# Performance work log

Measured on AMD Instinct MI355X. Metric: run time of the kernel, lower is better.

Reference implementation:

```python
import jax, jax.numpy as jnp
import numpy as np

EMBED_DIM = 1024
NUM_HEADS = 16
HEAD_DIM = EMBED_DIM // NUM_HEADS


def setup_inputs() -> dict:
    key = jax.random.key(0)
    ks = jax.random.split(key, 9)
    B, S, E, Hd = 1, 4096, EMBED_DIM, HEAD_DIM
    s = 0.02
    return {
        "x": jax.random.normal(ks[0], (B, S, E), jnp.float32),
        "mask": jnp.ones((B, S, S), jnp.int32),
        "Wq": jax.random.normal(ks[1], (E, E), jnp.float32) * s,
        "bq": jnp.zeros((E,), jnp.float32),
        "Wk": jax.random.normal(ks[2], (E, Hd), jnp.float32) * s,
        "bk": jnp.zeros((Hd,), jnp.float32),
        "Wv": jax.random.normal(ks[3], (E, Hd), jnp.float32) * s,
        "bv": jnp.zeros((Hd,), jnp.float32),
        "Wo": jax.random.normal(ks[4], (E, E), jnp.float32) * s,
        "bo": jnp.zeros((E,), jnp.float32),
    }


def reference(x, mask, Wq, bq, Wk, bk, Wv, bv, Wo, bo):
    B, S, E = x.shape
    H, Hd = NUM_HEADS, HEAD_DIM
    q = (x @ Wq + bq).reshape(B, S, H, Hd).transpose(0, 2, 1, 3)  # [B,H,S,Hd]
    k = x @ Wk + bk  # [B,S,Hd] single KV head (MQA)
    v = x @ Wv + bv  # [B,S,Hd]
    scale = 1.0 / np.sqrt(Hd).astype(np.float32)
    # broadcast single-head K across all query heads
    qk = jnp.einsum('bhqd,bkd->bhqk', q, k) * scale  # [B,H,S,S]
    qk = jnp.where(mask[:, None, :, :] == 0, jnp.float32(-10000.0), qk)
    attn = jax.nn.softmax(qk, axis=-1)
    out = jnp.einsum('bhqk,bkd->bhqd', attn, v)  # [B,H,S,Hd]
    out = out.transpose(0, 2, 1, 3).reshape(B, S, E)
    return out @ Wo + bo
```

## Files before the change

kernel.cpp:

```cpp
#include <hip/hip_runtime.h>
#include <hip/hip_bf16.h>
#include <stdint.h>

typedef __bf16 bf16x8 __attribute__((ext_vector_type(8)));
typedef float f32x4 __attribute__((ext_vector_type(4)));
typedef float f32x16 __attribute__((ext_vector_type(16)));
typedef unsigned int uint2v __attribute__((ext_vector_type(2)));

#define E_DIM 1024
#define HD 64
#define NH 16
#define QKV_LD 1152
#define LOG2E 1.44269504088896f

__device__ __forceinline__ float toF(float x) { return x; }
__device__ __forceinline__ float toF(__hip_bfloat16 x) { return __bfloat162float(x); }
__device__ __forceinline__ void storeOut(float* p, float v) { *p = v; }
__device__ __forceinline__ void storeOut(__hip_bfloat16* p, float v) { *p = __float2bfloat16(v); }

__device__ __forceinline__ unsigned cvtpk_bf16(float lo, float hi_) {
    unsigned r;
    asm("v_cvt_pk_bf16_f32 %0, %1, %2" : "=v"(r) : "v"(lo), "v"(hi_));
    return r;
}
__device__ __forceinline__ void perm32swap(unsigned& a, unsigned& b) {
    uint2v r = __builtin_amdgcn_permlane32_swap(a, b, false, false);
    a = r.x; b = r.y;
}
__device__ __forceinline__ float fexp2(float x) {
    float r;
    asm("v_exp_f32 %0, %1" : "=v"(r) : "v"(x));
    return r;
}

typedef __attribute__((address_space(1))) void gvoid;
typedef __attribute__((address_space(3))) void lvoid;
__device__ __forceinline__ void gload_lds16(const void* g, void* l) {
    __builtin_amdgcn_global_load_lds((gvoid*)g, (lvoid*)l, 16, 0, 0);
}

__global__ void cast_f32_bf16_kernel(const float* __restrict__ in, __hip_bfloat16* __restrict__ o, int n) {
    int i = (blockIdx.x * blockDim.x + threadIdx.x) * 4;
    if (i + 3 < n) {
        float4 v = *reinterpret_cast<const float4*>(in + i);
        __hip_bfloat16 t[4] = {__float2bfloat16(v.x), __float2bfloat16(v.y),
                               __float2bfloat16(v.z), __float2bfloat16(v.w)};
        *reinterpret_cast<uint2*>(o + i) = *reinterpret_cast<uint2*>(t);
    }
}

template<typename InT>
__global__ void transpose_cast_kernel(const InT* __restrict__ in, int ldi,
                                      __hip_bfloat16* __restrict__ out, int ldo,
                                      int R, int C) {
    __shared__ float tile[32][33];
    const int bx = blockIdx.x * 32;
    const int by = blockIdx.y * 32;
    const int tx = threadIdx.x & 31, ty = threadIdx.x >> 5;
#pragma unroll
    for (int j = 0; j < 4; ++j) {
        int r = bx + ty + j * 8, c = by + tx;
        tile[ty + j * 8][tx] = toF(in[(size_t)r * ldi + c]);
    }
    __syncthreads();
#pragma unroll
    for (int j = 0; j < 4; ++j) {
        int c = by + ty + j * 8, r = bx + tx;
        out[(size_t)c * ldo + r] = __float2bfloat16(tile[tx][ty + j * 8]);
    }
}

__global__ __launch_bounds__(256)
void transpose4_kernel(const float* __restrict__ Wq, const float* __restrict__ Wk,
                       const float* __restrict__ Wv, const float* __restrict__ Wo,
                       __hip_bfloat16* __restrict__ wqkvT, __hip_bfloat16* __restrict__ woT) {
    const int z = blockIdx.z;
    const float* in; __hip_bfloat16* out; int ldi;
    if (z == 0)      { in = Wq; out = wqkvT;                                ldi = E_DIM; }
    else if (z == 1) { if (blockIdx.y >= HD / 32) return;
                       in = Wk; out = wqkvT + (size_t)E_DIM * E_DIM;        ldi = HD; }
    else if (z == 2) { if (blockIdx.y >= HD / 32) return;
                       in = Wv; out = wqkvT + (size_t)(E_DIM + HD) * E_DIM; ldi = HD; }
    else             { in = Wo; out = woT;                                  ldi = E_DIM; }
    __shared__ float tile[32][33];
    const int bx = blockIdx.x * 32;
    const int by = blockIdx.y * 32;
    const int tx = threadIdx.x & 31, ty = threadIdx.x >> 5;
#pragma unroll
    for (int j = 0; j < 4; ++j) {
        int r = bx + ty + j * 8, c = by + tx;
        tile[ty + j * 8][tx] = in[(size_t)r * ldi + c];
    }
    __syncthreads();
#pragma unroll
    for (int j = 0; j < 4; ++j) {
        int c = by + ty + j * 8, r = bx + tx;
        out[(size_t)c * E_DIM + r] = __float2bfloat16(tile[tx][ty + j * 8]);
    }
}

__global__ void concat_bias3_kernel(const float* __restrict__ bq, const float* __restrict__ bk,
                                    const float* __restrict__ bv, float* __restrict__ bqkv) {
    int i = blockIdx.x * blockDim.x + threadIdx.x;
    if (i < E_DIM) bqkv[i] = bq[i];
    else if (i < E_DIM + HD) bqkv[i] = bk[i - E_DIM];
    else if (i < E_DIM + 2 * HD) bqkv[i] = bv[i - E_DIM - HD];
}

__global__ void maskbits_kernel(const int* __restrict__ mask, unsigned long long* __restrict__ mb,
                                int nwords) {
    int gtid = blockIdx.x * blockDim.x + threadIdx.x;
    int wid = gtid >> 6, lane = gtid & 63;
    int nw = (gridDim.x * blockDim.x) >> 6;
    for (int w = wid; w < nwords; w += nw) {
        int v = mask[(size_t)w * 64 + lane];
        unsigned long long b = __ballot(v != 0);
        if (lane == 0) mb[w] = b;
    }
}

template<typename OutT>
__global__ __launch_bounds__(256)
void gemm_bt3_kernel(const __hip_bfloat16* __restrict__ A,
                     const __hip_bfloat16* __restrict__ Bt,
                     const float* __restrict__ bias,
                     OutT* __restrict__ C,
                     int M, int N, int K, float sQ, int nQ, float sKV) {
    constexpr int BM = 64, BN = 128, BK = 64;
    __shared__ __align__(16) unsigned char lA[2][BM * BK * 2];
    __shared__ __align__(16) unsigned char lB[2][BN * BK * 2];
    const int ntn = N / BN;
    const int tm = blockIdx.x / ntn, tn = blockIdx.x % ntn;
    const int tid = threadIdx.x, lane = tid & 63, wave = tid >> 6;
    const int l15 = lane & 15, l4 = lane >> 4;
    const int wm = (wave >> 1) * 32, wn = (wave & 1) * 64;
    const int r0 = tm * BM, c0 = tn * BN;
    const int NK = K / BK;

    size_t aoff[2]; unsigned ldsoA[2];
    size_t boff[4]; unsigned ldsoB[4];
#pragma unroll
    for (int i = 0; i < 2; ++i) {
        int row = wave * 16 + i * 8 + (lane >> 3);
        int c = (lane & 7) ^ (row & 7);
        aoff[i] = (size_t)(r0 + row) * K * 2 + c * 16;
        ldsoA[i] = wave * 2048 + i * 1024;
    }
#pragma unroll
    for (int i = 0; i < 4; ++i) {
        int row = wave * 32 + i * 8 + (lane >> 3);
        int c = (lane & 7) ^ (row & 7);
        boff[i] = (size_t)(c0 + row) * K * 2 + c * 16;
        ldsoB[i] = wave * 4096 + i * 1024;
    }
    const char* Ab = (const char*)A;
    const char* Bb = (const char*)Bt;

#pragma unroll
    for (int i = 0; i < 2; ++i) gload_lds16(Ab + aoff[i], &lA[0][ldsoA[i]]);
#pragma unroll
    for (int i = 0; i < 4; ++i) gload_lds16(Bb + boff[i], &lB[0][ldsoB[i]]);
    __syncthreads();

    f32x4 z4 = {0.f, 0.f, 0.f, 0.f};
    f32x4 acc[2][4];
#pragma unroll
    for (int mi = 0; mi < 2; ++mi)
#pragma unroll
        for (int ni = 0; ni < 4; ++ni) acc[mi][ni] = z4;

    int buf = 0;
    for (int ks = 0; ks < NK; ++ks) {
        if (ks + 1 < NK) {
            size_t kb = (size_t)(ks + 1) * BK * 2;
#pragma unroll
            for (int i = 0; i < 2; ++i) gload_lds16(Ab + aoff[i] + kb, &lA[buf ^ 1][ldsoA[i]]);
#pragma unroll
            for (int i = 0; i < 4; ++i) gload_lds16(Bb + boff[i] + kb, &lB[buf ^ 1][ldsoB[i]]);
        }
        bf16x8 af[2][2], bf[4][2];
#pragma unroll
        for (int mi = 0; mi < 2; ++mi) {
            int row = wm + mi * 16 + l15;
#pragma unroll
            for (int kh = 0; kh < 2; ++kh) {
                int slot = (kh * 4 + l4) ^ (row & 7);
                af[mi][kh] = *reinterpret_cast<const bf16x8*>(&lA[buf][row * 128 + slot * 16]);
            }
        }
#pragma unroll
        for (int ni = 0; ni < 4; ++ni) {
            int row = wn + ni * 16 + l15;
#pragma unroll
            for (int kh = 0; kh < 2; ++kh) {
                int slot = (kh * 4 + l4) ^ (row & 7);
                bf[ni][kh] = *reinterpret_cast<const bf16x8*>(&lB[buf][row * 128 + slot * 16]);
            }
        }
        __builtin_amdgcn_s_setprio(1);
#pragma unroll
        for (int mi = 0; mi < 2; ++mi)
#pragma unroll
            for (int ni = 0; ni < 4; ++ni) {
                acc[mi][ni] = __builtin_amdgcn_mfma_f32_16x16x32_bf16(af[mi][0], bf[ni][0], acc[mi][ni], 0, 0, 0);
                acc[mi][ni] = __builtin_amdgcn_mfma_f32_16x16x32_bf16(af[mi][1], bf[ni][1], acc[mi][ni], 0, 0, 0);
            }
        __builtin_amdgcn_s_setprio(0);
        __syncthreads();
        buf ^= 1;
    }

#pragma unroll
    for (int ni = 0; ni < 4; ++ni) {
        int col = c0 + wn + ni * 16 + l15;
        float b = bias[col];
        float s = (col < nQ) ? sQ : sKV;
#pragma unroll
        for (int mi = 0; mi < 2; ++mi) {
            int row = r0 + wm + mi * 16 + l4 * 4;
#pragma unroll
            for (int r = 0; r < 4; ++r) {
                float v = (acc[mi][ni][r] + b) * s;
                storeOut(C + (size_t)(row + r) * N + col, v);
            }
        }
    }
}

__global__ __launch_bounds__(256, 2)
void mqa10_kernel(const __hip_bfloat16* __restrict__ qkv,
                  const __hip_bfloat16* __restrict__ vtb,
                  const unsigned long long* __restrict__ mbits,
                  __hip_bfloat16* __restrict__ attnb,
                  int S) {
    __shared__ __align__(16) unsigned char sKV[2][32768];
    const int tid = threadIdx.x, lane = tid & 63, w = tid >> 6;
    const int r31 = lane & 31, hi = lane >> 5, rx = r31 & 15;
    const int q0 = blockIdx.x * 32;
    const int h = blockIdx.y * 4 + w;
    const int NT = S / 128, NW64 = S / 64;
    const __hip_bfloat16* kvb = qkv + E_DIM;

    bf16x8 qf[4];
    {
        const __hip_bfloat16* qp = qkv + (size_t)(q0 + r31) * QKV_LD + h * HD + hi * 8;
#pragma unroll
        for (int s = 0; s < 4; ++s) qf[s] = *reinterpret_cast<const bf16x8*>(qp + 16 * s);
    }
    bf16x8 ones;
#pragma unroll
    for (int i = 0; i < 8; ++i) ones[i] = (__bf16)1.0f;

    const char* gbase[8];
    int gstep[8];
    unsigned ldsoff[8];
#pragma unroll
    for (int i = 0; i < 8; ++i) {
        int r = w * 32 + i * 4 + (lane >> 4);
        int sl = lane & 15;
        int c = sl ^ (r & 15);
        if (c < 8) {
            gbase[i] = (const char*)(kvb + (size_t)r * QKV_LD + c * 8);
            gstep[i] = 128 * QKV_LD * 2;
        } else {
            gbase[i] = (const char*)(vtb + (size_t)(r & 63) * S + (r >> 6) * 64 + (c - 8) * 8);
            gstep[i] = 128 * 2;
        }
        ldsoff[i] = w * 8192 + i * 1024;
    }

#pragma unroll
    for (int i = 0; i < 8; ++i) { gload_lds16(gbase[i], &sKV[0][ldsoff[i]]); gbase[i] += gstep[i]; }
    __syncthreads();

    f32x16 oacc[2], lacc;
#pragma unroll
    for (int i = 0; i < 16; ++i) { oacc[0][i] = 0.f; oacc[1][i] = 0.f; lacc[i] = 0.f; }

    const size_t mrow = (size_t)(q0 + r31) * NW64;
    int buf = 0;
    for (int t = 0; t < NT; ++t) {
        ulonglong2 wb = *reinterpret_cast<const ulonglong2*>(mbits + mrow + 2 * t);
        if (t + 1 < NT) {
#pragma unroll
            for (int i = 0; i < 8; ++i) { gload_lds16(gbase[i], &sKV[buf ^ 1][ldsoff[i]]); gbase[i] += gstep[i]; }
        }
        const unsigned char* bp = sKV[buf];

        f32x16 sacc[4];
        __builtin_amdgcn_s_setprio(1);
#pragma unroll
        for (int kb = 0; kb < 4; ++kb) {
            const unsigned char* rowp = bp + (kb * 32 + r31) * 256;
            f32x16 a;
#pragma unroll
            for (int i = 0; i < 16; ++i) a[i] = 0.f;
#pragma unroll
            for (int s = 0; s < 4; ++s) {
                int slot = (2 * s + hi) ^ rx;
                bf16x8 kf = *reinterpret_cast<const bf16x8*>(rowp + slot * 16);
                a = __builtin_amdgcn_mfma_f32_32x32x16_bf16(kf, qf[s], a, 0, 0, 0);
            }
            sacc[kb] = a;
        }
        __builtin_amdgcn_s_setprio(0);

        if ((wb.x & wb.y) != ~0ull) {
#pragma unroll
            for (int kb = 0; kb < 4; ++kb) {
                unsigned long long wv = (kb < 2) ? wb.x : wb.y;
                int base = (kb & 1) * 32;
#pragma unroll
                for (int r = 0; r < 16; ++r) {
                    int kl = base + (r & 3) + 8 * (r >> 2) + 4 * hi;
                    if (!((wv >> kl) & 1)) sacc[kb][r] = -14427.0f;
                }
            }
        }

#pragma unroll
        for (int kb = 0; kb < 4; ++kb)
#pragma unroll
            for (int r = 0; r < 16; ++r) sacc[kb][r] = fexp2(sacc[kb][r]);

#pragma unroll
        for (int j = 0; j < 2; ++j) {
            bf16x8 pa[4];
#pragma unroll
            for (int kk = 0; kk < 2; ++kk) {
#pragma unroll
                for (int half = 0; half < 2; ++half) {
                    int b0 = half * 8;
                    const f32x16& sv = sacc[2 * j + kk];
                    unsigned A = cvtpk_bf16(sv[b0 + 0], sv[b0 + 1]);
                    unsigned B = cvtpk_bf16(sv[b0 + 2], sv[b0 + 3]);
                    unsigned C = cvtpk_bf16(sv[b0 + 4], sv[b0 + 5]);
                    unsigned D = cvtpk_bf16(sv[b0 + 6], sv[b0 + 7]);
                    perm32swap(A, C);
                    perm32swap(B, D);
                    union { unsigned u[4]; bf16x8 v; } pk;
                    pk.u[0] = A; pk.u[1] = B; pk.u[2] = C; pk.u[3] = D;
                    pa[kk * 2 + half] = pk.v;
                }
            }
            __builtin_amdgcn_s_setprio(1);
#pragma unroll
            for (int db = 0; db < 2; ++db) {
                const unsigned char* rowp = bp + (j * 64 + db * 32 + r31) * 256;
                f32x16 a = oacc[db];
#pragma unroll
                for (int s = 0; s < 4; ++s) {
                    int slot = (8 + 2 * s + hi) ^ rx;
                    bf16x8 vf = *reinterpret_cast<const bf16x8*>(rowp + slot * 16);
                    a = __builtin_amdgcn_mfma_f32_32x32x16_bf16(vf, pa[s], a, 0, 0, 0);
                }
                oacc[db] = a;
            }
#pragma unroll
            for (int s = 0; s < 4; ++s)
                lacc = __builtin_amdgcn_mfma_f32_32x32x16_bf16(ones, pa[s], lacc, 0, 0, 0);
            __builtin_amdgcn_s_setprio(0);
        }

        __syncthreads();
        buf ^= 1;
    }

    float inv = 1.0f / lacc[0];
    __hip_bfloat16* op = attnb + (size_t)(q0 + r31) * E_DIM + h * HD;
#pragma unroll
    for (int db = 0; db < 2; ++db)
#pragma unroll
        for (int m = 0; m < 4; ++m) {
            uint2 pk;
            pk.x = cvtpk_bf16(oacc[db][4 * m + 0] * inv, oacc[db][4 * m + 1] * inv);
            pk.y = cvtpk_bf16(oacc[db][4 * m + 2] * inv, oacc[db][4 * m + 3] * inv);
            *reinterpret_cast<uint2*>(op + db * 32 + m * 8 + hi * 4) = pk;
        }
}

extern "C" void kernel_launch(void* const* d_in, const int* in_sizes, int n_in,
                              void* d_out, int out_size, void* d_ws, size_t ws_size,
                              hipStream_t stream) {
    (void)n_in; (void)out_size; (void)ws_size;
    const float* x  = (const float*)d_in[0];
    const int* mask = (const int*)d_in[1];
    const float* Wq = (const float*)d_in[2];
    const float* bq = (const float*)d_in[3];
    const float* Wk = (const float*)d_in[4];
    const float* bk = (const float*)d_in[5];
    const float* Wv = (const float*)d_in[6];
    const float* bv = (const float*)d_in[7];
    const float* Wo = (const float*)d_in[8];
    const float* bo = (const float*)d_in[9];
    float* out = (float*)d_out;

    const int E = E_DIM;
    const int S = in_sizes[0] / E;

    char* ws = (char*)d_ws;
    size_t off = 0;
    auto alloc = [&](size_t b) { char* p = ws + off; off += (b + 255) & ~(size_t)255; return p; };
    __hip_bfloat16* xb     = (__hip_bfloat16*)alloc((size_t)S * E * 2);
    __hip_bfloat16* wqkvT  = (__hip_bfloat16*)alloc((size_t)QKV_LD * E * 2);
    __hip_bfloat16* woT    = (__hip_bfloat16*)alloc((size_t)E * E * 2);
    __hip_bfloat16* qkvb   = (__hip_bfloat16*)alloc((size_t)S * QKV_LD * 2);
    __hip_bfloat16* vtb    = (__hip_bfloat16*)alloc((size_t)HD * S * 2);
    __hip_bfloat16* attnb  = (__hip_bfloat16*)alloc((size_t)S * E * 2);
    float* bqkv  = (float*)alloc(QKV_LD * 4);
    unsigned long long* mbits = (unsigned long long*)alloc((size_t)S * (S / 64) * 8);

    cast_f32_bf16_kernel<<<dim3((S * E / 4 + 255) / 256), dim3(256), 0, stream>>>(x, xb, S * E);
    transpose4_kernel<<<dim3(E / 32, E / 32, 4), dim3(256), 0, stream>>>(Wq, Wk, Wv, Wo, wqkvT, woT);
    concat_bias3_kernel<<<dim3((QKV_LD + 255) / 256), dim3(256), 0, stream>>>(bq, bk, bv, bqkv);
    maskbits_kernel<<<dim3(1024), dim3(256), 0, stream>>>(mask, mbits, S * (S / 64));

    gemm_bt3_kernel<__hip_bfloat16><<<dim3((S / 64) * (QKV_LD / 128)), dim3(256), 0, stream>>>(
        xb, wqkvT, bqkv, qkvb, S, QKV_LD, E, 0.125f * LOG2E, E, 1.0f);
    transpose_cast_kernel<__hip_bfloat16><<<dim3(S / 32, HD / 32), dim3(256), 0, stream>>>(
        qkvb + E + HD, QKV_LD, vtb, S, S, HD);
    mqa10_kernel<<<dim3(S / 32, NH / 4), dim3(256), 0, stream>>>(qkvb, vtb, mbits, attnb, S);
    gemm_bt3_kernel<float><<<dim3((S / 64) * (E / 128)), dim3(256), 0, stream>>>(
        attnb, woT, bo, out, S, E, E, 1.0f, E, 1.0f);
}
```

Baseline: 166.3 us.

## Split attention over KV range into two partial passes plus combine kernel

The attention kernel now splits the key/value sequence into two halves along a new grid dimension, with each block processing 64-key tiles instead of 128 and using half the shared memory. Unnormalized fp32 partial outputs and row sums go to a workspace, and a new combine kernel adds the two halves, normalizes, and writes bf16. The aim is more blocks and higher occupancy (launch bounds 3) for better latency hiding. The cost is extra fp32 global traffic of about 32MB, an additional launch, and more per-tile sync overhead from the smaller tiles.

```diff
diff --git a/kernel.cpp b/kernel.cpp
--- a/kernel.cpp
+++ b/kernel.cpp
@@ -11,6 +11,7 @@
 #define HD 64
 #define NH 16
 #define QKV_LD 1152
+#define KSPLIT 2
 #define LOG2E 1.44269504088896f
 
 __device__ __forceinline__ float toF(float x) { return x; }
@@ -227,18 +228,22 @@
     }
 }
 
-__global__ __launch_bounds__(256, 2)
-void mqa10_kernel(const __hip_bfloat16* __restrict__ qkv,
+__global__ __launch_bounds__(256, 3)
+void mqa11_kernel(const __hip_bfloat16* __restrict__ qkv,
                   const __hip_bfloat16* __restrict__ vtb,
                   const unsigned long long* __restrict__ mbits,
-                  __hip_bfloat16* __restrict__ attnb,
+                  float* __restrict__ po,
+                  float* __restrict__ ml,
                   int S) {
-    __shared__ __align__(16) unsigned char sKV[2][32768];
+    __shared__ __align__(16) unsigned char sKV[2][16384];
     const int tid = threadIdx.x, lane = tid & 63, w = tid >> 6;
     const int r31 = lane & 31, hi = lane >> 5, rx = r31 & 15;
     const int q0 = blockIdx.x * 32;
     const int h = blockIdx.y * 4 + w;
-    const int NT = S / 128, NW64 = S / 64;
+    const int split = blockIdx.z;
+    const int NW64 = S / 64;
+    const int NT = NW64 / KSPLIT;
+    const int k0base = split * (S / KSPLIT);
     const __hip_bfloat16* kvb = qkv + E_DIM;
 
     bf16x8 qf[4];
@@ -251,46 +256,46 @@
 #pragma unroll
     for (int i = 0; i < 8; ++i) ones[i] = (__bf16)1.0f;
 
-    const char* gbase[8];
-    int gstep[8];
-    unsigned ldsoff[8];
-#pragma unroll
-    for (int i = 0; i < 8; ++i) {
-        int r = w * 32 + i * 4 + (lane >> 4);
+    const char* gbase[4];
+    int gstep[4];
+    unsigned ldsoff[4];
+#pragma unroll
+    for (int i = 0; i < 4; ++i) {
+        int r = w * 16 + i * 4 + (lane >> 4);
         int sl = lane & 15;
         int c = sl ^ (r & 15);
         if (c < 8) {
-            gbase[i] = (const char*)(kvb + (size_t)r * QKV_LD + c * 8);
-            gstep[i] = 128 * QKV_LD * 2;
+            gbase[i] = (const char*)(kvb + (size_t)(k0base + r) * QKV_LD + c * 8);
+            gstep[i] = 64 * QKV_LD * 2;
         } else {
-            gbase[i] = (const char*)(vtb + (size_t)(r & 63) * S + (r >> 6) * 64 + (c - 8) * 8);
-            gstep[i] = 128 * 2;
-        }
-        ldsoff[i] = w * 8192 + i * 1024;
-    }
-
-#pragma unroll
-    for (int i = 0; i < 8; ++i) { gload_lds16(gbase[i], &sKV[0][ldsoff[i]]); gbase[i] += gstep[i]; }
+            gbase[i] = (const char*)(vtb + (size_t)r * S + k0base + (c - 8) * 8);
+            gstep[i] = 64 * 2;
+        }
+        ldsoff[i] = w * 4096 + i * 1024;
+    }
+
+#pragma unroll
+    for (int i = 0; i < 4; ++i) { gload_lds16(gbase[i], &sKV[0][ldsoff[i]]); gbase[i] += gstep[i]; }
     __syncthreads();
 
     f32x16 oacc[2], lacc;
 #pragma unroll
     for (int i = 0; i < 16; ++i) { oacc[0][i] = 0.f; oacc[1][i] = 0.f; lacc[i] = 0.f; }
 
-    const size_t mrow = (size_t)(q0 + r31) * NW64;
+    const size_t mrow = (size_t)(q0 + r31) * NW64 + (size_t)split * NT;
     int buf = 0;
     for (int t = 0; t < NT; ++t) {
-        ulonglong2 wb = *reinterpret_cast<const ulonglong2*>(mbits + mrow + 2 * t);
+        unsigned long long wb = mbits[mrow + t];
         if (t + 1 < NT) {
 #pragma unroll
-            for (int i = 0; i < 8; ++i) { gload_lds16(gbase[i], &sKV[buf ^ 1][ldsoff[i]]); gbase[i] += gstep[i]; }
+            for (int i = 0; i < 4; ++i) { gload_lds16(gbase[i], &sKV[buf ^ 1][ldsoff[i]]); gbase[i] += gstep[i]; }
         }
         const unsigned char* bp = sKV[buf];
 
-        f32x16 sacc[4];
+        f32x16 sacc[2];
         __builtin_amdgcn_s_setprio(1);
 #pragma unroll
-        for (int kb = 0; kb < 4; ++kb) {
+        for (int kb = 0; kb < 2; ++kb) {
             const unsigned char* rowp = bp + (kb * 32 + r31) * 256;
             f32x16 a;
 #pragma unroll
@@ -305,78 +310,90 @@
         }
         __builtin_amdgcn_s_setprio(0);
 
-        if ((wb.x & wb.y) != ~0ull) {
-#pragma unroll
-            for (int kb = 0; kb < 4; ++kb) {
-                unsigned long long wv = (kb < 2) ? wb.x : wb.y;
-                int base = (kb & 1) * 32;
+        if (wb != ~0ull) {
+#pragma unroll
+            for (int kb = 0; kb < 2; ++kb) {
+                int base = kb * 32;
 #pragma unroll
                 for (int r = 0; r < 16; ++r) {
                     int kl = base + (r & 3) + 8 * (r >> 2) + 4 * hi;
-                    if (!((wv >> kl) & 1)) sacc[kb][r] = -14427.0f;
+                    if (!((wb >> kl) & 1)) sacc[kb][r] = -14427.0f;
                 }
             }
         }
 
 #pragma unroll
-        for (int kb = 0; kb < 4; ++kb)
+        for (int kb = 0; kb < 2; ++kb)
 #pragma unroll
             for (int r = 0; r < 16; ++r) sacc[kb][r] = fexp2(sacc[kb][r]);
 
-#pragma unroll
-        for (int j = 0; j < 2; ++j) {
-            bf16x8 pa[4];
-#pragma unroll
-            for (int kk = 0; kk < 2; ++kk) {
-#pragma unroll
-                for (int half = 0; half < 2; ++half) {
-                    int b0 = half * 8;
-                    const f32x16& sv = sacc[2 * j + kk];
-                    unsigned A = cvtpk_bf16(sv[b0 + 0], sv[b0 + 1]);
-                    unsigned B = cvtpk_bf16(sv[b0 + 2], sv[b0 + 3]);
-                    unsigned C = cvtpk_bf16(sv[b0 + 4], sv[b0 + 5]);
-                    unsigned D = cvtpk_bf16(sv[b0 + 6], sv[b0 + 7]);
-                    perm32swap(A, C);
-                    perm32swap(B, D);
-                    union { unsigned u[4]; bf16x8 v; } pk;
-                    pk.u[0] = A; pk.u[1] = B; pk.u[2] = C; pk.u[3] = D;
-                    pa[kk * 2 + half] = pk.v;
-                }
-            }
-            __builtin_amdgcn_s_setprio(1);
-#pragma unroll
-            for (int db = 0; db < 2; ++db) {
-                const unsigned char* rowp = bp + (j * 64 + db * 32 + r31) * 256;
-                f32x16 a = oacc[db];
-#pragma unroll
-                for (int s = 0; s < 4; ++s) {
-                    int slot = (8 + 2 * s + hi) ^ rx;
-                    bf16x8 vf = *reinterpret_cast<const bf16x8*>(rowp + slot * 16);
-                    a = __builtin_amdgcn_mfma_f32_32x32x16_bf16(vf, pa[s], a, 0, 0, 0);
-                }
-                oacc[db] = a;
-            }
-#pragma unroll
-            for (int s = 0; s < 4; ++s)
-                lacc = __builtin_amdgcn_mfma_f32_32x32x16_bf16(ones, pa[s], lacc, 0, 0, 0);
-            __builtin_amdgcn_s_setprio(0);
-        }
+        bf16x8 pa[4];
+#pragma unroll
+        for (int kb = 0; kb < 2; ++kb) {
+#pragma unroll
+            for (int half = 0; half < 2; ++half) {
+                int b0 = half * 8;
+                const f32x16& sv = sacc[kb];
+                unsigned A = cvtpk_bf16(sv[b0 + 0], sv[b0 + 1]);
+                unsigned B = cvtpk_bf16(sv[b0 + 2], sv[b0 + 3]);
+                unsigned C = cvtpk_bf16(sv[b0 + 4], sv[b0 + 5]);
+                unsigned D = cvtpk_bf16(sv[b0 + 6], sv[b0 + 7]);
+                perm32swap(A, C);
+                perm32swap(B, D);
+                union { unsigned u[4]; bf16x8 v; } pk;
+                pk.u[0] = A; pk.u[1] = B; pk.u[2] = C; pk.u[3] = D;
+                pa[kb * 2 + half] = pk.v;
+            }
+        }
+
+        __builtin_amdgcn_s_setprio(1);
+#pragma unroll
+        for (int db = 0; db < 2; ++db) {
+            const unsigned char* rowp = bp + (db * 32 + r31) * 256;
+            f32x16 a = oacc[db];
+#pragma unroll
+            for (int s = 0; s < 4; ++s) {
+                int slot = (8 + 2 * s + hi) ^ rx;
+                bf16x8 vf = *reinterpret_cast<const bf16x8*>(rowp + slot * 16);
+                a = __builtin_amdgcn_mfma_f32_32x32x16_bf16(vf, pa[s], a, 0, 0, 0);
+            }
+            oacc[db] = a;
+        }
+#pragma unroll
+        for (int s = 0; s < 4; ++s)
+            lacc = __builtin_amdgcn_mfma_f32_32x32x16_bf16(ones, pa[s], lacc, 0, 0, 0);
+        __builtin_amdgcn_s_setprio(0);
 
         __syncthreads();
         buf ^= 1;
     }
 
-    float inv = 1.0f / lacc[0];
-    __hip_bfloat16* op = attnb + (size_t)(q0 + r31) * E_DIM + h * HD;
+    const int q = q0 + r31;
+    float* pop = po + (size_t)split * S * E_DIM + (size_t)q * E_DIM + h * HD;
 #pragma unroll
     for (int db = 0; db < 2; ++db)
 #pragma unroll
         for (int m = 0; m < 4; ++m) {
-            uint2 pk;
-            pk.x = cvtpk_bf16(oacc[db][4 * m + 0] * inv, oacc[db][4 * m + 1] * inv);
-            pk.y = cvtpk_bf16(oacc[db][4 * m + 2] * inv, oacc[db][4 * m + 3] * inv);
-            *reinterpret_cast<uint2*>(op + db * 32 + m * 8 + hi * 4) = pk;
-        }
+            float4 v4 = {oacc[db][4 * m + 0], oacc[db][4 * m + 1],
+                         oacc[db][4 * m + 2], oacc[db][4 * m + 3]};
+            *reinterpret_cast<float4*>(pop + db * 32 + m * 8 + hi * 4) = v4;
+        }
+    if (hi == 0) ml[((size_t)split * S + q) * NH + h] = lacc[0];
+}
+
+__global__ __launch_bounds__(256)
+void combine2_kernel(const float* __restrict__ po, const float* __restrict__ ml,
+                     __hip_bfloat16* __restrict__ attnb, int S) {
+    int i4 = (blockIdx.x * blockDim.x + threadIdx.x) * 4;
+    int q = i4 >> 10, h = (i4 & 1023) >> 6;
+    float l = ml[(size_t)q * NH + h] + ml[((size_t)S + q) * NH + h];
+    float4 a = *reinterpret_cast<const float4*>(po + i4);
+    float4 b = *reinterpret_cast<const float4*>(po + (size_t)S * E_DIM + i4);
+    float inv = 1.0f / l;
+    uint2 pk;
+    pk.x = cvtpk_bf16((a.x + b.x) * inv, (a.y + b.y) * inv);
+    pk.y = cvtpk_bf16((a.z + b.z) * inv, (a.w + b.w) * inv);
+    *reinterpret_cast<uint2*>(attnb + i4) = pk;
 }
 
 extern "C" void kernel_launch(void* const* d_in, const int* in_sizes, int n_in,
@@ -408,6 +425,8 @@
     __hip_bfloat16* vtb    = (__hip_bfloat16*)alloc((size_t)HD * S * 2);
     __hip_bfloat16* attnb  = (__hip_bfloat16*)alloc((size_t)S * E * 2);
     float* bqkv  = (float*)alloc(QKV_LD * 4);
+    float* po    = (float*)alloc((size_t)KSPLIT * S * E * 4);
+    float* ml    = (float*)alloc((size_t)KSPLIT * S * NH * 4);
     unsigned long long* mbits = (unsigned long long*)alloc((size_t)S * (S / 64) * 8);
 
     cast_f32_bf16_kernel<<<dim3((S * E / 4 + 255) / 256), dim3(256), 0, stream>>>(x, xb, S * E);
@@ -419,7 +438,9 @@
         xb, wqkvT, bqkv, qkvb, S, QKV_LD, E, 0.125f * LOG2E, E, 1.0f);
     transpose_cast_kernel<__hip_bfloat16><<<dim3(S / 32, HD / 32), dim3(256), 0, stream>>>(
         qkvb + E + HD, QKV_LD, vtb, S, S, HD);
-    mqa10_kernel<<<dim3(S / 32, NH / 4), dim3(256), 0, stream>>>(qkvb, vtb, mbits, attnb, S);
+    mqa11_kernel<<<dim3(S / 32, NH / 4, KSPLIT), dim3(256), 0, stream>>>(
+        qkvb, vtb, mbits, po, ml, S);
+    combine2_kernel<<<dim3(S * E / (256 * 4)), dim3(256), 0, stream>>>(po, ml, attnb, S);
     gemm_bt3_kernel<float><<<dim3((S / 64) * (E / 128)), dim3(256), 0, stream>>>(
         attnb, woT, bo, out, S, E, E, 1.0f, E, 1.0f);
 }
```

Result: slower. 224.2 us (+34.8%).

## Merge preprocessing kernels into one launch and fuse V transpose into QKV GEMM

Applied to the files above, without the earlier changes.

Folds the x cast, mask bit-packing, weight transposes and bias concat into a single block-partitioned prep kernel, so four launches become one. The separate V transpose kernel is removed: the QKV GEMM epilogue now also writes the V columns transposed into vtb. This cuts launch overhead and one read pass over qkv, at the cost of uncoalesced strided stores in the GEMM epilogue for the V tile blocks.

```diff
diff --git a/kernel.cpp b/kernel.cpp
--- a/kernel.cpp
+++ b/kernel.cpp
@@ -13,8 +13,6 @@
 #define QKV_LD 1152
 #define LOG2E 1.44269504088896f
 
-__device__ __forceinline__ float toF(float x) { return x; }
-__device__ __forceinline__ float toF(__hip_bfloat16 x) { return __bfloat162float(x); }
 __device__ __forceinline__ void storeOut(float* p, float v) { *p = v; }
 __device__ __forceinline__ void storeOut(__hip_bfloat16* p, float v) { *p = __float2bfloat16(v); }
 
@@ -39,92 +37,77 @@
     __builtin_amdgcn_global_load_lds((gvoid*)g, (lvoid*)l, 16, 0, 0);
 }
 
-__global__ void cast_f32_bf16_kernel(const float* __restrict__ in, __hip_bfloat16* __restrict__ o, int n) {
-    int i = (blockIdx.x * blockDim.x + threadIdx.x) * 4;
-    if (i + 3 < n) {
-        float4 v = *reinterpret_cast<const float4*>(in + i);
+__global__ __launch_bounds__(256)
+void prep_kernel(const float* __restrict__ x, __hip_bfloat16* __restrict__ xb,
+                 const int* __restrict__ mask, unsigned long long* __restrict__ mbits,
+                 const float* __restrict__ Wq, const float* __restrict__ Wk,
+                 const float* __restrict__ Wv, const float* __restrict__ Wo,
+                 __hip_bfloat16* __restrict__ wqkvT, __hip_bfloat16* __restrict__ woT,
+                 const float* __restrict__ bq, const float* __restrict__ bk,
+                 const float* __restrict__ bv, float* __restrict__ bqkv,
+                 int S) {
+    __shared__ float tile[32][33];
+    const int tid = threadIdx.x;
+    const int castBlocks = S * E_DIM / 1024;
+    const int maskBlocks = 1024;
+    int bid = blockIdx.x;
+
+    if (bid < castBlocks) {
+        int i = (bid * 256 + tid) * 4;
+        float4 v = *reinterpret_cast<const float4*>(x + i);
         __hip_bfloat16 t[4] = {__float2bfloat16(v.x), __float2bfloat16(v.y),
                                __float2bfloat16(v.z), __float2bfloat16(v.w)};
-        *reinterpret_cast<uint2*>(o + i) = *reinterpret_cast<uint2*>(t);
-    }
-}
-
-template<typename InT>
-__global__ void transpose_cast_kernel(const InT* __restrict__ in, int ldi,
-                                      __hip_bfloat16* __restrict__ out, int ldo,
-                                      int R, int C) {
-    __shared__ float tile[32][33];
-    const int bx = blockIdx.x * 32;
-    const int by = blockIdx.y * 32;
-    const int tx = threadIdx.x & 31, ty = threadIdx.x >> 5;
-#pragma unroll
-    for (int j = 0; j < 4; ++j) {
-        int r = bx + ty + j * 8, c = by + tx;
-        tile[ty + j * 8][tx] = toF(in[(size_t)r * ldi + c]);
-    }
-    __syncthreads();
-#pragma unroll
-    for (int j = 0; j < 4; ++j) {
-        int c = by + ty + j * 8, r = bx + tx;
-        out[(size_t)c * ldo + r] = __float2bfloat16(tile[tx][ty + j * 8]);
-    }
-}
-
-__global__ __launch_bounds__(256)
-void transpose4_kernel(const float* __restrict__ Wq, const float* __restrict__ Wk,
-                       const float* __restrict__ Wv, const float* __restrict__ Wo,
-                       __hip_bfloat16* __restrict__ wqkvT, __hip_bfloat16* __restrict__ woT) {
-    const int z = blockIdx.z;
-    const float* in; __hip_bfloat16* out; int ldi;
-    if (z == 0)      { in = Wq; out = wqkvT;                                ldi = E_DIM; }
-    else if (z == 1) { if (blockIdx.y >= HD / 32) return;
-                       in = Wk; out = wqkvT + (size_t)E_DIM * E_DIM;        ldi = HD; }
-    else if (z == 2) { if (blockIdx.y >= HD / 32) return;
-                       in = Wv; out = wqkvT + (size_t)(E_DIM + HD) * E_DIM; ldi = HD; }
-    else             { in = Wo; out = woT;                                  ldi = E_DIM; }
-    __shared__ float tile[32][33];
-    const int bx = blockIdx.x * 32;
-    const int by = blockIdx.y * 32;
-    const int tx = threadIdx.x & 31, ty = threadIdx.x >> 5;
-#pragma unroll
-    for (int j = 0; j < 4; ++j) {
-        int r = bx + ty + j * 8, c = by + tx;
-        tile[ty + j * 8][tx] = in[(size_t)r * ldi + c];
-    }
-    __syncthreads();
-#pragma unroll
-    for (int j = 0; j < 4; ++j) {
-        int c = by + ty + j * 8, r = bx + tx;
-        out[(size_t)c * E_DIM + r] = __float2bfloat16(tile[tx][ty + j * 8]);
-    }
-}
-
-__global__ void concat_bias3_kernel(const float* __restrict__ bq, const float* __restrict__ bk,
-                                    const float* __restrict__ bv, float* __restrict__ bqkv) {
-    int i = blockIdx.x * blockDim.x + threadIdx.x;
-    if (i < E_DIM) bqkv[i] = bq[i];
-    else if (i < E_DIM + HD) bqkv[i] = bk[i - E_DIM];
-    else if (i < E_DIM + 2 * HD) bqkv[i] = bv[i - E_DIM - HD];
-}
-
-__global__ void maskbits_kernel(const int* __restrict__ mask, unsigned long long* __restrict__ mb,
-                                int nwords) {
-    int gtid = blockIdx.x * blockDim.x + threadIdx.x;
-    int wid = gtid >> 6, lane = gtid & 63;
-    int nw = (gridDim.x * blockDim.x) >> 6;
-    for (int w = wid; w < nwords; w += nw) {
-        int v = mask[(size_t)w * 64 + lane];
-        unsigned long long b = __ballot(v != 0);
-        if (lane == 0) mb[w] = b;
-    }
-}
-
-template<typename OutT>
+        *reinterpret_cast<uint2*>(xb + i) = *reinterpret_cast<uint2*>(t);
+        return;
+    }
+    bid -= castBlocks;
+    if (bid < maskBlocks) {
+        int gtid = bid * 256 + tid;
+        int wid = gtid >> 6, lane = gtid & 63;
+        int nw = (maskBlocks * 256) >> 6;
+        int nwords = S * (S / 64);
+        for (int w = wid; w < nwords; w += nw) {
+            int v = mask[(size_t)w * 64 + lane];
+            unsigned long long b = __ballot(v != 0);
+            if (lane == 0) mbits[w] = b;
+        }
+        return;
+    }
+    bid -= maskBlocks;
+    if (bid < 2176) {
+        const float* in; __hip_bfloat16* out; int ldi, bx, by;
+        if (bid < 1024)      { in = Wq; out = wqkvT;                                ldi = E_DIM; bx = bid >> 5; by = bid & 31; }
+        else if (bid < 1088) { int t2 = bid - 1024;
+                               in = Wk; out = wqkvT + (size_t)E_DIM * E_DIM;        ldi = HD;    bx = t2 >> 1;  by = t2 & 1; }
+        else if (bid < 1152) { int t2 = bid - 1088;
+                               in = Wv; out = wqkvT + (size_t)(E_DIM + HD) * E_DIM; ldi = HD;    bx = t2 >> 1;  by = t2 & 1; }
+        else                 { int t2 = bid - 1152;
+                               in = Wo; out = woT;                                  ldi = E_DIM; bx = t2 >> 5; by = t2 & 31; }
+        const int tx = tid & 31, ty = tid >> 5;
+#pragma unroll
+        for (int j = 0; j < 4; ++j) {
+            int r = bx * 32 + ty + j * 8, c = by * 32 + tx;
+            tile[ty + j * 8][tx] = in[(size_t)r * ldi + c];
+        }
+        __syncthreads();
+#pragma unroll
+        for (int j = 0; j < 4; ++j) {
+            int c = by * 32 + ty + j * 8, r = bx * 32 + tx;
+            out[(size_t)c * E_DIM + r] = __float2bfloat16(tile[tx][ty + j * 8]);
+        }
+        return;
+    }
+    for (int i = tid; i < E_DIM + 2 * HD; i += 256)
+        bqkv[i] = (i < E_DIM) ? bq[i] : (i < E_DIM + HD ? bk[i - E_DIM] : bv[i - E_DIM - HD]);
+}
+
+template<typename OutT, bool VTB>
 __global__ __launch_bounds__(256)
 void gemm_bt3_kernel(const __hip_bfloat16* __restrict__ A,
                      const __hip_bfloat16* __restrict__ Bt,
                      const float* __restrict__ bias,
                      OutT* __restrict__ C,
+                     __hip_bfloat16* __restrict__ vtb,
                      int M, int N, int K, float sQ, int nQ, float sKV) {
     constexpr int BM = 64, BN = 128, BK = 64;
     __shared__ __align__(16) unsigned char lA[2][BM * BK * 2];
@@ -222,6 +205,10 @@
             for (int r = 0; r < 4; ++r) {
                 float v = (acc[mi][ni][r] + b) * s;
                 storeOut(C + (size_t)(row + r) * N + col, v);
+                if constexpr (VTB) {
+                    if (col >= nQ + HD)
+                        vtb[(size_t)(col - nQ - HD) * M + row + r] = __float2bfloat16(v);
+                }
             }
         }
     }
@@ -410,16 +397,13 @@
     float* bqkv  = (float*)alloc(QKV_LD * 4);
     unsigned long long* mbits = (unsigned long long*)alloc((size_t)S * (S / 64) * 8);
 
-    cast_f32_bf16_kernel<<<dim3((S * E / 4 + 255) / 256), dim3(256), 0, stream>>>(x, xb, S * E);
-    transpose4_kernel<<<dim3(E / 32, E / 32, 4), dim3(256), 0, stream>>>(Wq, Wk, Wv, Wo, wqkvT, woT);
-    concat_bias3_kernel<<<dim3((QKV_LD + 255) / 256), dim3(256), 0, stream>>>(bq, bk, bv, bqkv);
-    maskbits_kernel<<<dim3(1024), dim3(256), 0, stream>>>(mask, mbits, S * (S / 64));
-
-    gemm_bt3_kernel<__hip_bfloat16><<<dim3((S / 64) * (QKV_LD / 128)), dim3(256), 0, stream>>>(
-        xb, wqkvT, bqkv, qkvb, S, QKV_LD, E, 0.125f * LOG2E, E, 1.0f);
-    transpose_cast_kernel<__hip_bfloat16><<<dim3(S / 32, HD / 32), dim3(256), 0, stream>>>(
-        qkvb + E + HD, QKV_LD, vtb, S, S, HD);
+    const int prepBlocks = (S * E / 1024) + 1024 + 2176 + 1;
+    prep_kernel<<<dim3(prepBlocks), dim3(256), 0, stream>>>(
+        x, xb, mask, mbits, Wq, Wk, Wv, Wo, wqkvT, woT, bq, bk, bv, bqkv, S);
+
+    gemm_bt3_kernel<__hip_bfloat16, true><<<dim3((S / 64) * (QKV_LD / 128)), dim3(256), 0, stream>>>(
+        xb, wqkvT, bqkv, qkvb, vtb, S, QKV_LD, E, 0.125f * LOG2E, E, 1.0f);
     mqa10_kernel<<<dim3(S / 32, NH / 4), dim3(256), 0, stream>>>(qkvb, vtb, mbits, attnb, S);
-    gemm_bt3_kernel<float><<<dim3((S / 64) * (E / 128)), dim3(256), 0, stream>>>(
-        attnb, woT, bo, out, S, E, E, 1.0f, E, 1.0f);
-}
+    gemm_bt3_kernel<float, false><<<dim3((S / 64) * (E / 128)), dim3(256), 0, stream>>>(
+        attnb, woT, bo, out, nullptr, S, E, E, 1.0f, E, 1.0f);
+}
```

Result: faster. 158.6 us (median of 2 runs) (-4.6%).
